# Kernel optimization log

Measured on AMD Instinct MI355X. Metric: run time of the kernel, lower is better.

The kernel has to match this reference:

```python
import jax, jax.numpy as jnp
import numpy as np

N = 50000      # nodes
E = 1600000    # edges
L = 128        # latent_size


def _mlp(h, W1, b1, W2, b2):
    # MLP(in_dim, [L, L]) == Linear -> ReLU -> Linear
    return jax.nn.relu(h @ W1 + b1) @ W2 + b2


def setup_inputs() -> dict:
    key = jax.random.key(0)
    ks = jax.random.split(key, 12)
    glorot = lambda k, i, o: jax.random.normal(k, (i, o), jnp.float32) * (2.0 / (i + o)) ** 0.5
    return {
        "pos": jax.random.normal(ks[0], (N, 3), jnp.float32),
        "x": jax.random.normal(ks[1], (N, L), jnp.float32),
        "edge_attr": jax.random.normal(ks[2], (E, L), jnp.float32),
        "edge_index": jax.random.randint(ks[3], (2, E), 0, N, jnp.int64),
        "last_pred": jax.random.normal(ks[4], (N, 3), jnp.float32),
        "mask_idx": jax.random.randint(ks[5], (N, 1), 0, 2, jnp.int32).astype(bool),
        # pos_embedding MLP params (in=3)
        "Wp1": glorot(ks[6], 3, L), "bp1": jnp.zeros((L,), jnp.float32),
        "Wp2": glorot(ks[7], L, L), "bp2": jnp.zeros((L,), jnp.float32),
        # dis_embedding MLP params (in=1)
        "Wd1": glorot(ks[8], 1, L), "bd1": jnp.zeros((L,), jnp.float32),
        "Wd2": glorot(ks[9], L, L), "bd2": jnp.zeros((L,), jnp.float32),
    }


def reference(pos, x, edge_attr, edge_index, last_pred, mask_idx,
              Wp1, bp1, Wp2, bp2, Wd1, bd1, Wd2, bd2):
    # mode == 'mask': replace masked node positions with last prediction
    pos = jnp.where(mask_idx, last_pred, pos)                    # [N,3]
    extended_x = x + _mlp(pos, Wp1, bp1, Wp2, bp2)               # [N,L]
    row, col = edge_index[0], edge_index[1]
    diff = pos[row] - pos[col]                                   # [E,3]
    length = jnp.linalg.norm(diff, axis=-1, keepdims=True)       # [E,1]
    extended_edge_attr = edge_attr + _mlp(length, Wd1, bd1, Wd2, bd2)  # [E,L]
    return extended_x, extended_edge_attr
```

## Files before the change

kernel.cpp:

```cpp
#include <hip/hip_runtime.h>
#include <hip/hip_bf16.h>

#define NN 50000
#define EE 1600000
#define NB_NODE 391
#define NIV 129

typedef float f32x4 __attribute__((ext_vector_type(4)));
typedef __bf16 bf16x8 __attribute__((ext_vector_type(8)));

__device__ float gT[128];
__device__ __align__(16) float gA[NIV * 128];
__device__ __align__(16) float gB[NIV * 128];

__device__ __forceinline__ float edge_len(int e, const int* __restrict__ eidx,
                                          const float* __restrict__ pos,
                                          const float* __restrict__ lp,
                                          const int* __restrict__ msk) {
    int ri = eidx[e];
    int ci = eidx[EE + e];
    const float* pr = msk[ri] ? lp : pos;
    const float* pc = msk[ci] ? lp : pos;
    float dx = pr[3 * ri + 0] - pc[3 * ci + 0];
    float dy = pr[3 * ri + 1] - pc[3 * ci + 1];
    float dz = pr[3 * ri + 2] - pc[3 * ci + 2];
    return sqrtf(dx * dx + dy * dy + dz * dz);
}

union SM {
    struct {
        __bf16 w2l[16384];
        float w1l[384], b1l[128], b2l[128];
        float tbuf[8][512];
    } n;
    struct {
        float t_s[128];
        int   rank_s[128];
        float pa[4][128], pb[4][128];
    } p;
};

__device__ __forceinline__ void stage_w2(const float* __restrict__ W2, __bf16* w2l) {
    for (int idx = threadIdx.x; idx < 128 * 128; idx += 512) {
        int k = idx >> 7;
        int c = idx & 127;
        int dst = (((k >> 5) * 8 + (c >> 4)) * 64 + (((k >> 3) & 3) * 16 + (c & 15))) * 8 + (k & 7);
        w2l[dst] = (__bf16)W2[idx];
    }
}

__global__ __launch_bounds__(512, 3) void node_prep_kernel(
    const float* __restrict__ pos, const float* __restrict__ x,
    const float* __restrict__ lp, const int* __restrict__ msk,
    const float* __restrict__ Wp1, const float* __restrict__ bp1,
    const float* __restrict__ Wp2, const float* __restrict__ bp2,
    const float* __restrict__ Wd1, const float* __restrict__ bd1,
    const float* __restrict__ Wd2, const float* __restrict__ bd2,
    float* __restrict__ outx)
{
    __shared__ SM sm;

    if (blockIdx.x >= NB_NODE) {
        const int i = blockIdx.x - NB_NODE;
        const int c = threadIdx.x & 127;
        const int q = threadIdx.x >> 7;
        if (q == 0) {
            float w1 = Wd1[c], b1 = bd1[c];
            sm.p.t_s[c] = (w1 == 0.f) ? __builtin_inff() : (-b1 / w1);
        }
        __syncthreads();
        if (q == 0) {
            float t = sm.p.t_s[c];
            int rank = 0;
            for (int j = 0; j < 128; j++) {
                float tj = sm.p.t_s[j];
                rank += (tj < t) || (tj == t && j < c);
            }
            sm.p.rank_s[c] = rank;
            if (i == 0) gT[rank] = t;
        }
        __syncthreads();
        float a = 0.f, b = 0.f;
        for (int kk = 0; kk < 32; kk++) {
            int k = q * 32 + kk;
            float w1k = Wd1[k], b1k = bd1[k];
            bool act = (w1k > 0.f) ? (sm.p.rank_s[k] < i)
                     : (w1k < 0.f) ? (sm.p.rank_s[k] >= i)
                                   : (b1k > 0.f);
            if (act) {
                float w2 = Wd2[k * 128 + c];
                a = fmaf(w1k, w2, a);
                b = fmaf(b1k, w2, b);
            }
        }
        sm.p.pa[q][c] = a;
        sm.p.pb[q][c] = b;
        __syncthreads();
        if (q == 0) {
            float A = sm.p.pa[0][c] + sm.p.pa[1][c] + sm.p.pa[2][c] + sm.p.pa[3][c];
            float B = sm.p.pb[0][c] + sm.p.pb[1][c] + sm.p.pb[2][c] + sm.p.pb[3][c];
            gA[i * 128 + c] = A;
            gB[i * 128 + c] = B + bd2[c];
        }
        return;
    }

    stage_w2(Wp2, sm.n.w2l);
    for (int i = threadIdx.x; i < 384; i += 512) sm.n.w1l[i] = Wp1[i];
    if (threadIdx.x < 128) {
        sm.n.b1l[threadIdx.x] = bp1[threadIdx.x];
        sm.n.b2l[threadIdx.x] = bp2[threadIdx.x];
    }
    __syncthreads();

    const int w = threadIdx.x >> 6;
    const int l = threadIdx.x & 63;
    const int llo = l & 15;
    const int lgrp = l >> 4;
    float* tb = sm.n.tbuf[w];

    const int e0 = blockIdx.x * 128 + w * 16;
    const bool valid = (e0 + 16 <= NN);

    f32x4 ear[8];
    f32x4 acc[8];
    if (valid) {
        const float* srow = x + (size_t)e0 * 128;
#pragma unroll
        for (int j = 0; j < 8; j++) ear[j] = *(const f32x4*)(srow + j * 256 + l * 4);

        int nd = e0 + llo;
        const float* p = msk[nd] ? lp : pos;
        float px = p[3 * nd + 0];
        float py = p[3 * nd + 1];
        float pz = p[3 * nd + 2];

#pragma unroll
        for (int m = 0; m < 8; m++) acc[m] = (f32x4){0.f, 0.f, 0.f, 0.f};

#pragma unroll
        for (int kk = 0; kk < 4; kk++) {
            bf16x8 hf;
#pragma unroll
            for (int j = 0; j < 8; j++) {
                int k = kk * 32 + lgrp * 8 + j;
                float h = px * sm.n.w1l[k] + py * sm.n.w1l[128 + k]
                        + pz * sm.n.w1l[256 + k] + sm.n.b1l[k];
                hf[j] = (__bf16)fmaxf(h, 0.f);
            }
#pragma unroll
            for (int m = 0; m < 8; m++) {
                bf16x8 wf = *(const bf16x8*)&sm.n.w2l[((kk * 8 + m) * 64 + l) * 8];
                acc[m] = __builtin_amdgcn_mfma_f32_16x16x32_bf16(wf, hf, acc[m], 0, 0, 0);
            }
        }
    }

    float* drow = outx + (size_t)e0 * 128;
    f32x4 b2v = *(const f32x4*)&sm.n.b2l[(l & 31) * 4];

#pragma unroll
    for (int p = 0; p < 4; p++) {
        if (valid && (llo >> 2) == p) {
            int r = llo & 3;
#pragma unroll
            for (int m = 0; m < 8; m++) {
                int c = (m * 16 + lgrp * 4 + r * 4) & 127;
                *(f32x4*)&tb[r * 128 + c] = acc[m];
            }
        }
        __syncthreads();
        if (valid) {
#pragma unroll
            for (int i = 0; i < 2; i++) {
                int row = 2 * i + (l >> 5);
                int c = ((l & 31) * 4 + row * 4) & 127;
                f32x4 tv = *(const f32x4*)&tb[row * 128 + c];
                f32x4 o = tv + b2v + ear[p * 2 + i];
                *(f32x4*)(drow + p * 512 + i * 256 + l * 4) = o;
            }
        }
        __syncthreads();
    }
}

__global__ __launch_bounds__(256) void leniv_kernel(
    const int* __restrict__ eidx, const float* __restrict__ pos,
    const float* __restrict__ lp, const int* __restrict__ msk,
    float2* __restrict__ lenivp)
{
    __shared__ float ts[128];
    if (threadIdx.x < 128) ts[threadIdx.x] = gT[threadIdx.x];
    __syncthreads();
    int e = blockIdx.x * 256 + threadIdx.x;
    if (e < EE) {
        float lv = edge_len(e, eidx, pos, lp, msk);
        int lo = 0;
#pragma unroll
        for (int s = 128; s > 0; s >>= 1) {
            int m = lo + s;
            if (m <= 128 && ts[m - 1] < lv) lo = m;
        }
        lenivp[e] = make_float2(lv, (float)lo);
    }
}

template <bool PRE>
__global__ __launch_bounds__(256) void edge_kernel(
    const float* __restrict__ ea, const float2* __restrict__ lenivp,
    const int* __restrict__ eidx, const float* __restrict__ pos,
    const float* __restrict__ lp, const int* __restrict__ msk,
    float* __restrict__ oute)
{
    __shared__ float ts[128];
    if (!PRE) {
        if (threadIdx.x < 128) ts[threadIdx.x] = gT[threadIdx.x];
        __syncthreads();
    }

    const int w  = threadIdx.x >> 6;
    const int l  = threadIdx.x & 63;
    const int c4 = (l & 31) * 4;
    const int rh = l >> 5;

    for (int base = blockIdx.x * 32 + w * 8; base < EE; base += gridDim.x * 32) {
        f32x4 e[4];
#pragma unroll
        for (int j = 0; j < 4; j++)
            e[j] = *(const f32x4*)(ea + (size_t)(base + 2 * j) * 128 + l * 4);

        float lenv[4];
        int iv[4];
#pragma unroll
        for (int j = 0; j < 4; j++) {
            int r = base + 2 * j + rh;
            if (PRE) {
                float2 f2 = lenivp[r];
                lenv[j] = f2.x;
                iv[j] = (int)f2.y;
            } else {
                lenv[j] = edge_len(r, eidx, pos, lp, msk);
                int lo = 0;
#pragma unroll
                for (int s = 128; s > 0; s >>= 1) {
                    int m = lo + s;
                    if (m <= 128 && ts[m - 1] < lenv[j]) lo = m;
                }
                iv[j] = lo;
            }
        }

#pragma unroll
        for (int j = 0; j < 4; j++) {
            const f32x4 a = *(const f32x4*)&gA[iv[j] * 128 + c4];
            const f32x4 b = *(const f32x4*)&gB[iv[j] * 128 + c4];
            *(f32x4*)(oute + (size_t)(base + 2 * j) * 128 + l * 4) =
                e[j] + (lenv[j] * a + b);
        }
    }
}

extern "C" void kernel_launch(void* const* d_in, const int* in_sizes, int n_in,
                              void* d_out, int out_size, void* d_ws, size_t ws_size,
                              hipStream_t stream) {
    const float* pos        = (const float*)d_in[0];
    const float* x          = (const float*)d_in[1];
    const float* edge_attr  = (const float*)d_in[2];
    const int* edge_index   = (const int*)d_in[3];
    const float* last_pred  = (const float*)d_in[4];
    const int* mask         = (const int*)d_in[5];
    const float* Wp1 = (const float*)d_in[6];
    const float* bp1 = (const float*)d_in[7];
    const float* Wp2 = (const float*)d_in[8];
    const float* bp2 = (const float*)d_in[9];
    const float* Wd1 = (const float*)d_in[10];
    const float* bd1 = (const float*)d_in[11];
    const float* Wd2 = (const float*)d_in[12];
    const float* bd2 = (const float*)d_in[13];

    float* outx = (float*)d_out;
    float* oute = outx + (size_t)NN * 128;

    node_prep_kernel<<<NB_NODE + NIV, 512, 0, stream>>>(
        pos, x, last_pred, mask,
        Wp1, bp1, Wp2, bp2, Wd1, bd1, Wd2, bd2, outx);

    if (ws_size >= (size_t)EE * 8) {
        float2* lenivp = (float2*)d_ws;
        leniv_kernel<<<(EE + 255) / 256, 256, 0, stream>>>(
            edge_index, pos, last_pred, mask, lenivp);
        edge_kernel<true><<<2048, 256, 0, stream>>>(
            edge_attr, lenivp, edge_index, pos, last_pred, mask, oute);
    } else {
        edge_kernel<false><<<2048, 256, 0, stream>>>(
            edge_attr, nullptr, edge_index, pos, last_pred, mask, oute);
    }
}
```

Before: 368.1 us.

## Fuse edge-length/interval computation into the node setup kernel launch

Moves the per-edge length and breakpoint-interval search into extra blocks of the node prep kernel. Those blocks recompute the sorted ReLU breakpoints locally rather than reading them from the global table the node blocks write, so the separate kernel launch and its dependency on the prior launch go away. The edge kernel now reads two edges' length/interval pairs with one 16-byte load instead of two float2 loads. The added blocks share the large-LDS, 512-thread launch configuration, which may limit occupancy for the simple edge work.

```diff
diff --git a/kernel.cpp b/kernel.cpp
--- a/kernel.cpp
+++ b/kernel.cpp
@@ -5,6 +5,8 @@
 #define EE 1600000
 #define NB_NODE 391
 #define NIV 129
+#define NB_LENIV 3125
+#define NB_EDGE 2048
 
 typedef float f32x4 __attribute__((ext_vector_type(4)));
 typedef __bf16 bf16x8 __attribute__((ext_vector_type(8)));
@@ -38,6 +40,10 @@
         int   rank_s[128];
         float pa[4][128], pb[4][128];
     } p;
+    struct {
+        float t_s[128];
+        float ts[128];
+    } v;
 };
 
 __device__ __forceinline__ void stage_w2(const float* __restrict__ W2, __bf16* w2l) {
@@ -49,16 +55,46 @@
     }
 }
 
-__global__ __launch_bounds__(512, 3) void node_prep_kernel(
+__global__ __launch_bounds__(512, 3) void setup_kernel(
     const float* __restrict__ pos, const float* __restrict__ x,
+    const int* __restrict__ eidx,
     const float* __restrict__ lp, const int* __restrict__ msk,
     const float* __restrict__ Wp1, const float* __restrict__ bp1,
     const float* __restrict__ Wp2, const float* __restrict__ bp2,
     const float* __restrict__ Wd1, const float* __restrict__ bd1,
     const float* __restrict__ Wd2, const float* __restrict__ bd2,
-    float* __restrict__ outx)
+    float* __restrict__ outx, float2* __restrict__ lenivp)
 {
     __shared__ SM sm;
+
+    if (blockIdx.x >= NB_NODE + NIV) {
+        if (threadIdx.x < 128) {
+            float w1 = Wd1[threadIdx.x], b1 = bd1[threadIdx.x];
+            sm.v.t_s[threadIdx.x] = (w1 == 0.f) ? __builtin_inff() : (-b1 / w1);
+        }
+        __syncthreads();
+        if (threadIdx.x < 128) {
+            float t = sm.v.t_s[threadIdx.x];
+            int rank = 0;
+            for (int j = 0; j < 128; j++) {
+                float tj = sm.v.t_s[j];
+                rank += (tj < t) || (tj == t && j < (int)threadIdx.x);
+            }
+            sm.v.ts[rank] = t;
+        }
+        __syncthreads();
+
+        int e = (blockIdx.x - (NB_NODE + NIV)) * 512 + threadIdx.x;
+        float lv = edge_len(e, eidx, pos, lp, msk);
+        int lo = 0;
+#pragma unroll
+        for (int s = 128; s > 0; s >>= 1) {
+            int m = lo + s;
+            if (m <= 128 && sm.v.ts[m - 1] < lv) lo = m;
+        }
+        lenivp[e] = make_float2(lv, (float)lo);
+        return;
+    }
 
     if (blockIdx.x >= NB_NODE) {
         const int i = blockIdx.x - NB_NODE;
@@ -184,27 +220,6 @@
     }
 }
 
-__global__ __launch_bounds__(256) void leniv_kernel(
-    const int* __restrict__ eidx, const float* __restrict__ pos,
-    const float* __restrict__ lp, const int* __restrict__ msk,
-    float2* __restrict__ lenivp)
-{
-    __shared__ float ts[128];
-    if (threadIdx.x < 128) ts[threadIdx.x] = gT[threadIdx.x];
-    __syncthreads();
-    int e = blockIdx.x * 256 + threadIdx.x;
-    if (e < EE) {
-        float lv = edge_len(e, eidx, pos, lp, msk);
-        int lo = 0;
-#pragma unroll
-        for (int s = 128; s > 0; s >>= 1) {
-            int m = lo + s;
-            if (m <= 128 && ts[m - 1] < lv) lo = m;
-        }
-        lenivp[e] = make_float2(lv, (float)lo);
-    }
-}
-
 template <bool PRE>
 __global__ __launch_bounds__(256) void edge_kernel(
     const float* __restrict__ ea, const float2* __restrict__ lenivp,
@@ -233,12 +248,12 @@
         int iv[4];
 #pragma unroll
         for (int j = 0; j < 4; j++) {
-            int r = base + 2 * j + rh;
             if (PRE) {
-                float2 f2 = lenivp[r];
-                lenv[j] = f2.x;
-                iv[j] = (int)f2.y;
+                f32x4 li = *(const f32x4*)&lenivp[base + 2 * j];
+                lenv[j] = rh ? li.z : li.x;
+                iv[j]   = (int)(rh ? li.w : li.y);
             } else {
+                int r = base + 2 * j + rh;
                 lenv[j] = edge_len(r, eidx, pos, lp, msk);
                 int lo = 0;
 #pragma unroll
@@ -281,18 +296,20 @@
     float* outx = (float*)d_out;
     float* oute = outx + (size_t)NN * 128;
 
-    node_prep_kernel<<<NB_NODE + NIV, 512, 0, stream>>>(
-        pos, x, last_pred, mask,
-        Wp1, bp1, Wp2, bp2, Wd1, bd1, Wd2, bd2, outx);
-
     if (ws_size >= (size_t)EE * 8) {
         float2* lenivp = (float2*)d_ws;
-        leniv_kernel<<<(EE + 255) / 256, 256, 0, stream>>>(
-            edge_index, pos, last_pred, mask, lenivp);
-        edge_kernel<true><<<2048, 256, 0, stream>>>(
+
+        setup_kernel<<<NB_NODE + NIV + NB_LENIV, 512, 0, stream>>>(
+            pos, x, edge_index, last_pred, mask,
+            Wp1, bp1, Wp2, bp2, Wd1, bd1, Wd2, bd2, outx, lenivp);
+
+        edge_kernel<true><<<NB_EDGE, 256, 0, stream>>>(
             edge_attr, lenivp, edge_index, pos, last_pred, mask, oute);
     } else {
-        edge_kernel<false><<<2048, 256, 0, stream>>>(
+        setup_kernel<<<NB_NODE + NIV, 512, 0, stream>>>(
+            pos, x, edge_index, last_pred, mask,
+            Wp1, bp1, Wp2, bp2, Wd1, bd1, Wd2, bd2, outx, nullptr);
+        edge_kernel<false><<<NB_EDGE, 256, 0, stream>>>(
             edge_attr, nullptr, edge_index, pos, last_pred, mask, oute);
     }
 }
```

Result: slower. 386.8 us (+5.1%).
